# Kernel tuning notes

Hardware: AMD Instinct MI355X
Metric: run time of the kernel (lower is better)

## Reference

```python
import jax, jax.numpy as jnp
import numpy as np
import math

N_VERT = 35709
N_FACE = 70789
BATCH = 32


def _normalize(x, axis=-1, eps=1e-12):
    n = jnp.linalg.norm(x, axis=axis, keepdims=True)
    return x / jnp.maximum(n, eps)


def setup_inputs() -> dict:
    key = jax.random.key(0)
    ks = jax.random.split(key, 9)
    coeff = jax.random.normal(ks[0], (BATCH, 277), jnp.float32)
    idBase = jax.random.normal(ks[1], (3 * N_VERT, 80), jnp.float32)
    exBase = jax.random.normal(ks[2], (3 * N_VERT, 64), jnp.float32)
    texBase = jax.random.normal(ks[3], (3 * N_VERT, 100), jnp.float32)
    meanshape = jax.random.normal(ks[4], (3 * N_VERT,), jnp.float32)
    meantex = jax.random.normal(ks[5], (3 * N_VERT,), jnp.float32)
    face_buf = jax.random.randint(ks[6], (N_FACE, 3), 0, N_VERT, jnp.int32)
    # point_buf may index the appended zero-normal row at position N_FACE (padding)
    point_buf = jax.random.randint(ks[7], (N_VERT, 8), 0, N_FACE + 1, jnp.int32)
    keypoints = jax.random.randint(ks[8], (68,), 0, N_VERT, jnp.int32)
    return dict(coeff=coeff, idBase=idBase, exBase=exBase, texBase=texBase,
                meanshape=meanshape, meantex=meantex, face_buf=face_buf,
                point_buf=point_buf, keypoints=keypoints)


def reference(coeff, idBase, exBase, texBase, meanshape, meantex,
              face_buf, point_buf, keypoints):
    B = coeff.shape[0]
    # ---- Split_coeff (canonical 80/64/100/3/27/3 layout) ----
    id_c = coeff[:, :80]
    ex_c = coeff[:, 80:144]
    tex_c = coeff[:, 144:244]
    angles = coeff[:, 244:247]
    gamma = coeff[:, 247:274]
    trans = coeff[:, 274:277]
    cam_scale = jnp.ones((B, 1), coeff.dtype)
    f_scale = jnp.ones((B, 1), coeff.dtype)

    # ---- Shape formation ----
    fs = (jnp.einsum('ij,aj->ai', idBase, id_c)
          + jnp.einsum('ij,aj->ai', exBase, ex_c)
          + meanshape[None, :])
    fs = fs.reshape(B, -1, 3)  # [B, N, 3]
    fs = fs - jnp.mean(meanshape.reshape(-1, 3), axis=0)[None, None, :]

    # ---- Texture formation ----
    tex = (jnp.einsum('ij,aj->ai', texBase, tex_c) + meantex[None, :]).reshape(B, -1, 3)

    # ---- Rotation matrix (Rz @ Ry @ Rx, then transpose) ----
    cx, sx = jnp.cos(angles[:, 0]), jnp.sin(angles[:, 0])
    cy, sy = jnp.cos(angles[:, 1]), jnp.sin(angles[:, 1])
    cz, sz = jnp.cos(angles[:, 2]), jnp.sin(angles[:, 2])
    o, z = jnp.ones_like(cx), jnp.zeros_like(cx)
    Rx = jnp.stack([o, z, z, z, cx, -sx, z, sx, cx], -1).reshape(B, 3, 3)
    Ry = jnp.stack([cy, z, sy, z, o, z, -sy, z, cy], -1).reshape(B, 3, 3)
    Rz = jnp.stack([cz, -sz, z, sz, cz, z, z, z, o], -1).reshape(B, 3, 3)
    rot = jnp.swapaxes(jnp.matmul(jnp.matmul(Rz, Ry), Rx), 1, 2)  # [B,3,3]

    # ---- Compute_norm: gather face verts, cross, aggregate to vertices ----
    v1 = fs[:, face_buf[:, 0], :]  # [B, F, 3]
    v2 = fs[:, face_buf[:, 1], :]
    v3 = fs[:, face_buf[:, 2], :]
    face_norm = _normalize(jnp.cross(v1 - v2, v2 - v3), axis=2)  # [B, F, 3]
    face_norm = jnp.concatenate(
        [face_norm, jnp.zeros((B, 1, 3), face_norm.dtype)], axis=1)  # pad row
    v_norm = _normalize(jnp.sum(face_norm[:, point_buf, :], axis=2), axis=2)  # [B,N,3]

    norm_r = jnp.matmul(v_norm, rot)

    # ---- Rigid transform + landmarks ----
    fst = jnp.matmul(fs, rot) + trans[:, None, :]
    lm = fst[:, keypoints, :]  # [B, 68, 3]

    # ---- Projection block (applied to landmarks) ----
    focal = 1015.0 * f_scale  # [B,1]
    camera_pos = jnp.array([0.0, 0.0, 10.0], coeff.dtype) * cam_scale[:, :, None]  # [B,1,3]
    reverse_z = jnp.diag(jnp.array([1.0, 1.0, -1.0], coeff.dtype))
    z1 = jnp.zeros((B, 1), coeff.dtype)
    z2 = jnp.zeros((B, 2), coeff.dtype)
    o1 = jnp.ones((B, 1), coeff.dtype)
    p_matrix = jnp.concatenate(
        [focal, z1, 112.0 * o1, z1, focal, 112.0 * o1, z2, o1], axis=1).reshape(B, 3, 3)
    lm_cam = jnp.matmul(lm, reverse_z[None]) + camera_pos
    aug = jnp.matmul(lm_cam, jnp.swapaxes(p_matrix, 1, 2))
    landmark_p = aug[..., :2] / aug[..., 2:3]

    # ---- SH illumination ----
    init_lit = jnp.array([0.8, 0, 0, 0, 0, 0, 0, 0, 0], coeff.dtype)
    g = gamma.reshape(B, 3, 9) + init_lit[None, None, :]
    pi = math.pi
    a0, a1, a2 = pi, 2 * pi / math.sqrt(3.0), 2 * pi / math.sqrt(8.0)
    c0 = 1.0 / math.sqrt(4 * pi)
    c1 = math.sqrt(3.0) / math.sqrt(4 * pi)
    c2 = 3 * math.sqrt(5.0) / math.sqrt(12 * pi)
    nx, ny, nz = norm_r[..., 0], norm_r[..., 1], norm_r[..., 2]
    Y = jnp.stack([
        a0 * c0 * jnp.ones_like(nx),
        -a1 * c1 * ny,
        a1 * c1 * nz,
        -a1 * c1 * nx,
        a2 * c2 * nx * ny,
        -a2 * c2 * ny * nz,
        a2 * c2 * 0.5 / math.sqrt(3.0) * (3 * nz * nz - 1),
        -a2 * c2 * nx * nz,
        a2 * c2 * 0.5 * (nx * nx - ny * ny),
    ], axis=-1)  # [B, N, 9]
    lighting = jnp.einsum('bnk,bck->bnc', Y, g)  # [B, N, 3]
    face_color = tex * lighting

    return face_color, landmark_p, fst
```

## Files before the change

### kernel.cpp

```cpp
#include <hip/hip_runtime.h>

#define N_VERT 35709
#define N_FACE 70789
#define NB 32
#define M3 (3*N_VERT)

#define WS_FS4X  ((size_t)0)
#define WS_FN4X  (WS_FS4X + (size_t)N_VERT*128)
#define WS_CPAD  (WS_FN4X + (size_t)(N_FACE+1)*128)
#define WS_ROT   (WS_CPAD + (size_t)NB*256)
#define WS_TRE   (WS_ROT + (size_t)NB*9)
#define WS_G     (WS_TRE + (size_t)NB*3)
#define WS_MEAN  (WS_G + (size_t)NB*27)

#define FC_OFF   ((size_t)0)
#define LM_OFF   ((size_t)NB*M3)
#define FST_OFF  (LM_OFF + (size_t)NB*68*2)

#define A0C0 0.88622692545275801f
#define A1C1 1.77245385090551603f
#define A2C2 2.42703239430f
#define Y6C  0.70062393935f
#define Y8C  1.21351619715f

__global__ void __launch_bounds__(256) face3d_stageA1(
    const float* __restrict__ ms, float* __restrict__ ws) {
  float s0=0.f, s1=0.f, s2=0.f;
  for (int v = blockIdx.x*256 + threadIdx.x; v < N_VERT; v += gridDim.x*256) {
    s0 += ms[3*v+0]; s1 += ms[3*v+1]; s2 += ms[3*v+2];
  }
  #pragma unroll
  for (int off = 32; off > 0; off >>= 1) {
    s0 += __shfl_down(s0, off);
    s1 += __shfl_down(s1, off);
    s2 += __shfl_down(s2, off);
  }
  if ((threadIdx.x & 63) == 0) {
    atomicAdd(&ws[WS_MEAN+0], s0);
    atomicAdd(&ws[WS_MEAN+1], s1);
    atomicAdd(&ws[WS_MEAN+2], s2);
  }
}

__global__ void __launch_bounds__(256) face3d_stageA2(
    const float* __restrict__ coeff, float* __restrict__ ws) {
  int t = threadIdx.x;
  float m0 = ws[WS_MEAN+0]*(1.0f/N_VERT);
  float m1 = ws[WS_MEAN+1]*(1.0f/N_VERT);
  float m2 = ws[WS_MEAN+2]*(1.0f/N_VERT);
  for (int idx = t; idx < NB*256; idx += 256) {
    int b = idx >> 8, k = idx & 255;
    ws[WS_CPAD + idx] = (k < 244) ? coeff[b*277 + k] : 0.0f;
  }
  for (int idx = t; idx < NB*27; idx += 256) {
    int b = idx / 27, k = idx - b*27;
    ws[WS_G + idx] = coeff[b*277 + 247 + k] + (((k % 9) == 0) ? 0.8f : 0.0f);
  }
  if (t < NB) {
    int b = t;
    float ax = coeff[b*277+244], ay = coeff[b*277+245], az = coeff[b*277+246];
    float cx=cosf(ax), sx=sinf(ax);
    float cy=cosf(ay), sy=sinf(ay);
    float cz=cosf(az), sz=sinf(az);
    float T00=cz*cy, T01=-sz, T02=cz*sy;
    float T10=sz*cy, T11=cz,  T12=sz*sy;
    float T20=-sy,   T21=0.f, T22=cy;
    float R[3][3];
    R[0][0]=T00; R[0][1]=T01*cx+T02*sx; R[0][2]=-T01*sx+T02*cx;
    R[1][0]=T10; R[1][1]=T11*cx+T12*sx; R[1][2]=-T11*sx+T12*cx;
    R[2][0]=T20; R[2][1]=T21*cx+T22*sx; R[2][2]=-T21*sx+T22*cx;
    float rot[3][3];
    #pragma unroll
    for (int c=0;c<3;c++)
      #pragma unroll
      for (int j=0;j<3;j++)
        rot[c][j] = R[j][c];
    #pragma unroll
    for (int c=0;c<3;c++)
      #pragma unroll
      for (int j=0;j<3;j++)
        ws[WS_ROT + b*9 + c*3 + j] = rot[c][j];
    #pragma unroll
    for (int j=0;j<3;j++)
      ws[WS_TRE + b*3 + j] = coeff[b*277+274+j]
        - (m0*rot[0][j] + m1*rot[1][j] + m2*rot[2][j]);
  }
}

template<int NK4, int COFF>
__device__ __forceinline__ void phaseK(const float* __restrict__ Arow,
                                       const float4* __restrict__ Wl,
                                       float* __restrict__ acc) {
  const float4* __restrict__ A = (const float4*)Arow;
  float4 cur = A[0];
  #pragma unroll 1
  for (int s = 0; s < NK4; ++s) {
    float4 a = cur;
    if (s + 1 < NK4) cur = A[s+1];
    #pragma unroll
    for (int b = 0; b < NB; ++b) {
      float4 w = Wl[b*64 + COFF + s];
      acc[b] = fmaf(a.x, w.x, fmaf(a.y, w.y, fmaf(a.z, w.z, fmaf(a.w, w.w, acc[b]))));
    }
  }
}

__global__ void __launch_bounds__(256) face3d_stageB(
    const float* __restrict__ idB, const float* __restrict__ exB,
    const float* __restrict__ texB, const float* __restrict__ meanshape,
    const float* __restrict__ meantex, const float* __restrict__ cpad,
    float* __restrict__ fs4x, float* __restrict__ texOut) {
  __shared__ float4 W[2048];
  int t = threadIdx.x;
  {
    const float4* __restrict__ src = (const float4*)cpad;
    #pragma unroll
    for (int j = 0; j < 8; ++j) W[t + 256*j] = src[t + 256*j];
  }
  __syncthreads();
  int r = blockIdx.x*256 + t;
  if (r >= M3) return;

  float acc[NB];
  #pragma unroll
  for (int b=0;b<NB;b++) acc[b]=0.f;
  phaseK<20, 0 >(idB + (size_t)r*80,  W, acc);
  phaseK<16, 20>(exB + (size_t)r*64,  W, acc);
  {
    float ms = meanshape[r];
    int v = r/3, c = r - 3*v;
    float* dst = fs4x + (size_t)v*128 + c;
    #pragma unroll
    for (int b=0;b<NB;b++) dst[b*4] = acc[b] + ms;
  }
  #pragma unroll
  for (int b=0;b<NB;b++) acc[b]=0.f;
  phaseK<25, 36>(texB + (size_t)r*100, W, acc);
  {
    float mt = meantex[r];
    #pragma unroll
    for (int b=0;b<NB;b++) texOut[(size_t)b*M3 + r] = acc[b] + mt;
  }
}

__global__ void __launch_bounds__(256) face3d_stageC(
    const int* __restrict__ face_buf, const float* __restrict__ fs4x,
    float* __restrict__ fn4x) {
  int t = threadIdx.x;
  int b = t & 31, fi = t >> 5;
  int f = blockIdx.x*8 + fi;
  if (f > N_FACE) return;
  float4* o = (float4*)(fn4x + ((size_t)f*32 + b)*4);
  if (f == N_FACE) { *o = make_float4(0.f,0.f,0.f,0.f); return; }
  int i0 = face_buf[f*3+0];
  int i1 = face_buf[f*3+1];
  int i2 = face_buf[f*3+2];
  float4 p1 = *(const float4*)(fs4x + ((size_t)i0*32 + b)*4);
  float4 p2 = *(const float4*)(fs4x + ((size_t)i1*32 + b)*4);
  float4 p3 = *(const float4*)(fs4x + ((size_t)i2*32 + b)*4);
  float e1x = p1.x-p2.x, e1y = p1.y-p2.y, e1z = p1.z-p2.z;
  float e2x = p2.x-p3.x, e2y = p2.y-p3.y, e2z = p2.z-p3.z;
  float nx = e1y*e2z - e1z*e2y;
  float ny = e1z*e2x - e1x*e2z;
  float nz = e1x*e2y - e1y*e2x;
  float inv = 1.0f / fmaxf(sqrtf(nx*nx + ny*ny + nz*nz), 1e-12f);
  *o = make_float4(nx*inv, ny*inv, nz*inv, 0.f);
}

__global__ void __launch_bounds__(256) face3d_stageD(
    const int* __restrict__ point_buf, const int* __restrict__ keypoints,
    const float* __restrict__ fs4x, const float* __restrict__ fn4x,
    const float* __restrict__ rotAll, const float* __restrict__ treAll,
    const float* __restrict__ gAll, float* __restrict__ out) {
  const int mainBlocks = (N_VERT + 7)/8;
  int bid = blockIdx.x;
  int t = threadIdx.x;
  if (bid < mainBlocks) {
    __shared__ float rotL[NB*9];
    __shared__ float treL[NB*3];
    __shared__ float gL[NB*27];
    __shared__ float fstL[NB*33];
    __shared__ float LL[NB*33];
    if (t < NB*9)  rotL[t] = rotAll[t];
    if (t < NB*3)  treL[t] = treAll[t];
    for (int i = t; i < NB*27; i += 256) gL[i] = gAll[i];
    __syncthreads();
    int b = t & 31, vi = t >> 5;
    int v0 = bid*8;
    int v = v0 + vi;
    if (v < N_VERT) {
      const int4 pb0 = *(const int4*)(point_buf + (size_t)v*8);
      const int4 pb1 = *(const int4*)(point_buf + (size_t)v*8 + 4);
      float4 g0 = *(const float4*)(fn4x + ((size_t)pb0.x*32 + b)*4);
      float4 g1 = *(const float4*)(fn4x + ((size_t)pb0.y*32 + b)*4);
      float4 g2 = *(const float4*)(fn4x + ((size_t)pb0.z*32 + b)*4);
      float4 g3 = *(const float4*)(fn4x + ((size_t)pb0.w*32 + b)*4);
      float4 g4 = *(const float4*)(fn4x + ((size_t)pb1.x*32 + b)*4);
      float4 g5 = *(const float4*)(fn4x + ((size_t)pb1.y*32 + b)*4);
      float4 g6 = *(const float4*)(fn4x + ((size_t)pb1.z*32 + b)*4);
      float4 g7 = *(const float4*)(fn4x + ((size_t)pb1.w*32 + b)*4);
      float sx = ((g0.x+g1.x)+(g2.x+g3.x)) + ((g4.x+g5.x)+(g6.x+g7.x));
      float sy = ((g0.y+g1.y)+(g2.y+g3.y)) + ((g4.y+g5.y)+(g6.y+g7.y));
      float sz = ((g0.z+g1.z)+(g2.z+g3.z)) + ((g4.z+g5.z)+(g6.z+g7.z));
      float inv = 1.0f / fmaxf(sqrtf(sx*sx + sy*sy + sz*sz), 1e-12f);
      float n0 = sx*inv, n1 = sy*inv, n2 = sz*inv;
      const float* rot = rotL + b*9;
      float r00=rot[0], r01=rot[1], r02=rot[2];
      float r10=rot[3], r11=rot[4], r12=rot[5];
      float r20=rot[6], r21=rot[7], r22=rot[8];
      float nx = n0*r00 + n1*r10 + n2*r20;
      float ny = n0*r01 + n1*r11 + n2*r21;
      float nz = n0*r02 + n1*r12 + n2*r22;
      float Y1 = -A1C1*ny;
      float Y2 =  A1C1*nz;
      float Y3 = -A1C1*nx;
      float Y4 =  A2C2*nx*ny;
      float Y5 = -A2C2*ny*nz;
      float Y6 =  Y6C*(3.f*nz*nz - 1.f);
      float Y7 = -A2C2*nx*nz;
      float Y8 =  Y8C*(nx*nx - ny*ny);
      const float* g = gL + b*27;
      #pragma unroll
      for (int c = 0; c < 3; ++c) {
        const float* gc = g + c*9;
        float Lc = A0C0*gc[0] + Y1*gc[1] + Y2*gc[2] + Y3*gc[3] + Y4*gc[4]
                 + Y5*gc[5] + Y6*gc[6] + Y7*gc[7] + Y8*gc[8];
        LL[b*33 + vi*4 + c] = Lc;
      }
      float4 fsv = *(const float4*)(fs4x + ((size_t)v*32 + b)*4);
      const float* tre = treL + b*3;
      fstL[b*33 + vi*4 + 0] = fsv.x*r00 + fsv.y*r10 + fsv.z*r20 + tre[0];
      fstL[b*33 + vi*4 + 1] = fsv.x*r01 + fsv.y*r11 + fsv.z*r21 + tre[1];
      fstL[b*33 + vi*4 + 2] = fsv.x*r02 + fsv.y*r12 + fsv.z*r22 + tre[2];
    }
    __syncthreads();
    int b2 = t >> 3, w = t & 7;
    if (v0 + w < N_VERT) {
      size_t obase = (size_t)b2*M3 + (size_t)(v0 + w)*3;
      float f0 = fstL[b2*33 + w*4 + 0];
      float f1 = fstL[b2*33 + w*4 + 1];
      float f2 = fstL[b2*33 + w*4 + 2];
      out[FST_OFF + obase + 0] = f0;
      out[FST_OFF + obase + 1] = f1;
      out[FST_OFF + obase + 2] = f2;
      float l0 = LL[b2*33 + w*4 + 0];
      float l1 = LL[b2*33 + w*4 + 1];
      float l2 = LL[b2*33 + w*4 + 2];
      float t0 = out[FC_OFF + obase + 0];
      float t1 = out[FC_OFF + obase + 1];
      float t2 = out[FC_OFF + obase + 2];
      out[FC_OFF + obase + 0] = t0*l0;
      out[FC_OFF + obase + 1] = t1*l1;
      out[FC_OFF + obase + 2] = t2*l2;
    }
  } else {
    int idx = (bid - mainBlocks)*256 + t;
    if (idx >= NB*68) return;
    int b = idx & 31, j = idx >> 5;
    int kp = keypoints[j];
    const float* rot = rotAll + b*9;
    const float* tre = treAll + b*3;
    float4 fsv = *(const float4*)(fs4x + ((size_t)kp*32 + b)*4);
    float o0 = fsv.x*rot[0] + fsv.y*rot[3] + fsv.z*rot[6] + tre[0];
    float o1 = fsv.x*rot[1] + fsv.y*rot[4] + fsv.z*rot[7] + tre[1];
    float o2 = fsv.x*rot[2] + fsv.y*rot[5] + fsv.z*rot[8] + tre[2];
    float zc = 10.0f - o2;
    float axv = 1015.0f*o0 + 112.0f*zc;
    float ayv = 1015.0f*o1 + 112.0f*zc;
    out[LM_OFF + (size_t)b*136 + (size_t)j*2 + 0] = axv/zc;
    out[LM_OFF + (size_t)b*136 + (size_t)j*2 + 1] = ayv/zc;
  }
}

extern "C" void kernel_launch(void* const* d_in, const int* in_sizes, int n_in,
                              void* d_out, int out_size, void* d_ws, size_t ws_size,
                              hipStream_t stream) {
  const float* coeff     = (const float*)d_in[0];
  const float* idB       = (const float*)d_in[1];
  const float* exB       = (const float*)d_in[2];
  const float* texB      = (const float*)d_in[3];
  const float* meanshape = (const float*)d_in[4];
  const float* meantex   = (const float*)d_in[5];
  const int*   face_buf  = (const int*)d_in[6];
  const int*   point_buf = (const int*)d_in[7];
  const int*   keypoints = (const int*)d_in[8];
  float* out = (float*)d_out;
  float* ws  = (float*)d_ws;

  hipMemsetAsync((char*)d_ws + WS_MEAN*sizeof(float), 0, 3*sizeof(float), stream);

  hipLaunchKernelGGL(face3d_stageA1, dim3(56), dim3(256), 0, stream, meanshape, ws);
  hipLaunchKernelGGL(face3d_stageA2, dim3(1), dim3(256), 0, stream, coeff, ws);

  int gridB = (M3 + 255)/256;
  hipLaunchKernelGGL(face3d_stageB, dim3(gridB), dim3(256), 0, stream,
                     idB, exB, texB, meanshape, meantex,
                     ws + WS_CPAD, ws + WS_FS4X, out + FC_OFF);

  int gridC = (N_FACE + 1 + 7)/8;
  hipLaunchKernelGGL(face3d_stageC, dim3(gridC), dim3(256), 0, stream,
                     face_buf, ws + WS_FS4X, ws + WS_FN4X);

  int mainBlocks = (N_VERT + 7)/8;
  int lmBlocks   = (NB*68 + 255)/256;
  hipLaunchKernelGGL(face3d_stageD, dim3(mainBlocks + lmBlocks), dim3(256), 0, stream,
                     point_buf, keypoints, ws + WS_FS4X, ws + WS_FN4X,
                     ws + WS_ROT, ws + WS_TRE, ws + WS_G, out);
}
```

Baseline: 286.5 us.

## Stream basis rows through double-buffered LDS with async global-to-LDS loads

Stage B is restructured so each block stages tiles of the basis matrices and coefficients into double-buffered LDS using global_load_lds, with explicit vmcnt waits and barriers. Each thread now computes a 4-row by 8-batch register tile instead of one row across all 32 batches. Shape (id+ex) and texture work are split across separate blocks, which doubles the grid. The intent is coalesced, overlapped streaming of the roughly 100 MB of basis data and more parallelism, in exchange for hand-tuned waitcnt logic that is fragile.

```diff
diff --git a/kernel.cpp b/kernel.cpp
--- a/kernel.cpp
+++ b/kernel.cpp
@@ -87,20 +87,57 @@
   }
 }
 
-template<int NK4, int COFF>
-__device__ __forceinline__ void phaseK(const float* __restrict__ Arow,
-                                       const float4* __restrict__ Wl,
-                                       float* __restrict__ acc) {
-  const float4* __restrict__ A = (const float4*)Arow;
-  float4 cur = A[0];
-  #pragma unroll 1
-  for (int s = 0; s < NK4; ++s) {
-    float4 a = cur;
-    if (s + 1 < NK4) cur = A[s+1];
-    #pragma unroll
-    for (int b = 0; b < NB; ++b) {
-      float4 w = Wl[b*64 + COFF + s];
-      acc[b] = fmaf(a.x, w.x, fmaf(a.y, w.y, fmaf(a.z, w.z, fmaf(a.w, w.w, acc[b]))));
+
+__device__ __forceinline__ void gload16(const void* g, void* l) {
+  __builtin_amdgcn_global_load_lds((const __attribute__((address_space(1))) void*)g,
+                                   (__attribute__((address_space(3))) void*)l, 16, 0, 0);
+}
+
+#define B_SYNC() do { __builtin_amdgcn_sched_barrier(0); \
+                      __builtin_amdgcn_s_barrier(); \
+                      __builtin_amdgcn_sched_barrier(0); } while (0)
+#define B_WAIT(N) do { __builtin_amdgcn_sched_barrier(0); \
+                       asm volatile("s_waitcnt vmcnt(" #N ")"); \
+                       B_SYNC(); } while (0)
+
+template<int KT4>
+__device__ __forceinline__ void stageB_stage(const float* __restrict__ A, int K4,
+                                             int gk4, const float* __restrict__ cpad,
+                                             int wk4, int r0, int t,
+                                             float4* __restrict__ buf) {
+  #pragma unroll
+  for (int p = 0; p < KT4; ++p) {
+    int i = p*256 + t;
+    int row = i / KT4;
+    int s4 = i - row*KT4;
+    int gr = r0 + row; gr = (gr < M3) ? gr : (M3-1);
+    gload16(A + ((size_t)gr*K4 + gk4 + s4)*4, buf + i);
+  }
+  {
+    int b = t / KT4;
+    int s4 = t - b*KT4;
+    if (b >= NB) { b = NB-1; s4 = KT4-1; }
+    gload16(cpad + ((size_t)b*64 + wk4 + s4)*4, buf + 256*KT4 + t);
+  }
+}
+
+template<int KT4>
+__device__ __forceinline__ void stageB_compute(const float4* __restrict__ buf,
+                                               int bg8, int lane, float acc[4][8]) {
+  const float4* __restrict__ Wl = buf + 256*KT4;
+  #pragma unroll
+  for (int s4 = 0; s4 < KT4; ++s4) {
+    float4 a0 = buf[(lane      )*KT4 + s4];
+    float4 a1 = buf[(lane +  64)*KT4 + s4];
+    float4 a2 = buf[(lane + 128)*KT4 + s4];
+    float4 a3 = buf[(lane + 192)*KT4 + s4];
+    #pragma unroll
+    for (int bb = 0; bb < 8; ++bb) {
+      float4 w = Wl[(bg8 + bb)*KT4 + s4];
+      acc[0][bb] = fmaf(a0.w, w.w, fmaf(a0.z, w.z, fmaf(a0.y, w.y, fmaf(a0.x, w.x, acc[0][bb]))));
+      acc[1][bb] = fmaf(a1.w, w.w, fmaf(a1.z, w.z, fmaf(a1.y, w.y, fmaf(a1.x, w.x, acc[1][bb]))));
+      acc[2][bb] = fmaf(a2.w, w.w, fmaf(a2.z, w.z, fmaf(a2.y, w.y, fmaf(a2.x, w.x, acc[2][bb]))));
+      acc[3][bb] = fmaf(a3.w, w.w, fmaf(a3.z, w.z, fmaf(a3.y, w.y, fmaf(a3.x, w.x, acc[3][bb]))));
     }
   }
 }
@@ -110,36 +147,80 @@
     const float* __restrict__ texB, const float* __restrict__ meanshape,
     const float* __restrict__ meantex, const float* __restrict__ cpad,
     float* __restrict__ fs4x, float* __restrict__ texOut) {
-  __shared__ float4 W[2048];
+  __shared__ float4 lds[2][1536];
   int t = threadIdx.x;
-  {
-    const float4* __restrict__ src = (const float4*)cpad;
-    #pragma unroll
-    for (int j = 0; j < 8; ++j) W[t + 256*j] = src[t + 256*j];
-  }
-  __syncthreads();
-  int r = blockIdx.x*256 + t;
-  if (r >= M3) return;
-
-  float acc[NB];
+  int lane = t & 63;
+  int bg8 = (t >> 6) << 3;
+  int bid = blockIdx.x;
+  int r0 = (bid >> 1) * 256;
+
+  float acc[4][8];
   #pragma unroll
-  for (int b=0;b<NB;b++) acc[b]=0.f;
-  phaseK<20, 0 >(idB + (size_t)r*80,  W, acc);
-  phaseK<16, 20>(exB + (size_t)r*64,  W, acc);
-  {
-    float ms = meanshape[r];
-    int v = r/3, c = r - 3*v;
-    float* dst = fs4x + (size_t)v*128 + c;
-    #pragma unroll
-    for (int b=0;b<NB;b++) dst[b*4] = acc[b] + ms;
-  }
-  #pragma unroll
-  for (int b=0;b<NB;b++) acc[b]=0.f;
-  phaseK<25, 36>(texB + (size_t)r*100, W, acc);
-  {
-    float mt = meantex[r];
-    #pragma unroll
-    for (int b=0;b<NB;b++) texOut[(size_t)b*M3 + r] = acc[b] + mt;
+  for (int j = 0; j < 4; ++j)
+    #pragma unroll
+    for (int bb = 0; bb < 8; ++bb) acc[j][bb] = 0.f;
+
+  float4* buf0 = &lds[0][0];
+  float4* buf1 = &lds[1][0];
+
+  if ((bid & 1) == 0) {
+    stageB_stage<5>(idB, 20, 0, cpad, 0, r0, t, buf0);
+    #pragma unroll 1
+    for (int tt = 0; tt < 7; ++tt) {
+      int nt = tt + 1;
+      float4* nb = (tt & 1) ? buf0 : buf1;
+      if (nt < 7) {
+        const float* An = (nt < 4) ? idB : exB;
+        int K4n = (nt < 4) ? 20 : 16;
+        int g4n = (nt < 4) ? nt*5 : (nt-4)*5;
+        stageB_stage<5>(An, K4n, g4n, cpad, nt*5, r0, t, nb);
+        B_WAIT(6);
+      } else {
+        stageB_stage<1>(exB, 16, 15, cpad, 35, r0, t, nb);
+        B_WAIT(2);
+      }
+      stageB_compute<5>((tt & 1) ? buf1 : buf0, bg8, lane, acc);
+      B_SYNC();
+    }
+    B_WAIT(0);
+    stageB_compute<1>(buf1, bg8, lane, acc);
+    #pragma unroll
+    for (int j = 0; j < 4; ++j) {
+      int r = r0 + lane + 64*j;
+      if (r < M3) {
+        float ms = meanshape[r];
+        int v = r / 3;
+        int c = r - 3*v;
+        float* dst = fs4x + (size_t)v*128 + c;
+        #pragma unroll
+        for (int bb = 0; bb < 8; ++bb)
+          dst[(bg8 + bb)*4] = acc[j][bb] + ms;
+      }
+    }
+  } else {
+    stageB_stage<5>(texB, 25, 0, cpad, 36, r0, t, buf0);
+    #pragma unroll 1
+    for (int tt = 0; tt < 5; ++tt) {
+      if (tt < 4) {
+        stageB_stage<5>(texB, 25, (tt+1)*5, cpad, 36 + (tt+1)*5, r0, t,
+                        (tt & 1) ? buf0 : buf1);
+        B_WAIT(6);
+      } else {
+        B_WAIT(0);
+      }
+      stageB_compute<5>((tt & 1) ? buf1 : buf0, bg8, lane, acc);
+      if (tt < 4) B_SYNC();
+    }
+    #pragma unroll
+    for (int j = 0; j < 4; ++j) {
+      int r = r0 + lane + 64*j;
+      if (r < M3) {
+        float mt = meantex[r];
+        #pragma unroll
+        for (int bb = 0; bb < 8; ++bb)
+          texOut[(size_t)(bg8 + bb)*M3 + r] = acc[j][bb] + mt;
+      }
+    }
   }
 }
 
@@ -292,7 +373,7 @@
   hipLaunchKernelGGL(face3d_stageA1, dim3(56), dim3(256), 0, stream, meanshape, ws);
   hipLaunchKernelGGL(face3d_stageA2, dim3(1), dim3(256), 0, stream, coeff, ws);
 
-  int gridB = (M3 + 255)/256;
+  int gridB = 2 * ((M3 + 255)/256);
   hipLaunchKernelGGL(face3d_stageB, dim3(gridB), dim3(256), 0, stream,
                      idB, exB, texB, meanshape, meantex,
                      ws + WS_CPAD, ws + WS_FS4X, out + FC_OFF);
```

New measurement: 289.0 us. About the same (+0.9%).

## Split stage B GEMV into shape/tex blocks with 4-way K-split per row

Applied to the files above, without the earlier changes.

Stage B now runs separate blocks for the shape (id+ex) and texture products. Within a block, each group of four threads splits the K dimension of one output row, and partial sums are combined with two rounds of xor shuffles so each lane writes 8 batch outputs. The aim is more blocks and waves in flight, shorter per-thread dependent loops, and more coalesced base-matrix reads. In exchange it adds shuffle traffic, and the shared weight table is reloaded by every block.

```diff
diff --git a/kernel.cpp b/kernel.cpp
--- a/kernel.cpp
+++ b/kernel.cpp
@@ -87,59 +87,110 @@
   }
 }
 
-template<int NK4, int COFF>
-__device__ __forceinline__ void phaseK(const float* __restrict__ Arow,
-                                       const float4* __restrict__ Wl,
-                                       float* __restrict__ acc) {
-  const float4* __restrict__ A = (const float4*)Arow;
-  float4 cur = A[0];
-  #pragma unroll 1
-  for (int s = 0; s < NK4; ++s) {
-    float4 a = cur;
-    if (s + 1 < NK4) cur = A[s+1];
-    #pragma unroll
-    for (int b = 0; b < NB; ++b) {
-      float4 w = Wl[b*64 + COFF + s];
-      acc[b] = fmaf(a.x, w.x, fmaf(a.y, w.y, fmaf(a.z, w.z, fmaf(a.w, w.w, acc[b]))));
-    }
-  }
-}
 
 __global__ void __launch_bounds__(256) face3d_stageB(
     const float* __restrict__ idB, const float* __restrict__ exB,
     const float* __restrict__ texB, const float* __restrict__ meanshape,
     const float* __restrict__ meantex, const float* __restrict__ cpad,
     float* __restrict__ fs4x, float* __restrict__ texOut) {
-  __shared__ float4 W[2048];
+  __shared__ float4 Wl[NB*36];
   int t = threadIdx.x;
-  {
-    const float4* __restrict__ src = (const float4*)cpad;
-    #pragma unroll
-    for (int j = 0; j < 8; ++j) W[t + 256*j] = src[t + 256*j];
+  int bid = blockIdx.x;
+  int isTex = bid & 1;
+  int r0 = (bid >> 1) * 64;
+  int rl = t >> 2, q = t & 3;
+  int r = r0 + rl;
+  int rc = (r < M3) ? r : (M3-1);
+
+  const float4* __restrict__ cp4 = (const float4*)cpad;
+  if (!isTex) {
+    for (int i = t; i < NB*36; i += 256) {
+      int b = i / 36, j = i - b*36;
+      Wl[i] = cp4[b*64 + j];
+    }
+  } else {
+    for (int i = t; i < NB*25; i += 256) {
+      int b = i / 25, j = i - b*25;
+      Wl[i] = cp4[b*64 + 36 + j];
+    }
   }
   __syncthreads();
-  int r = blockIdx.x*256 + t;
-  if (r >= M3) return;
 
   float acc[NB];
   #pragma unroll
-  for (int b=0;b<NB;b++) acc[b]=0.f;
-  phaseK<20, 0 >(idB + (size_t)r*80,  W, acc);
-  phaseK<16, 20>(exB + (size_t)r*64,  W, acc);
-  {
-    float ms = meanshape[r];
-    int v = r/3, c = r - 3*v;
-    float* dst = fs4x + (size_t)v*128 + c;
-    #pragma unroll
-    for (int b=0;b<NB;b++) dst[b*4] = acc[b] + ms;
-  }
+  for (int b = 0; b < NB; ++b) acc[b] = 0.f;
+
+  if (!isTex) {
+    const float4* __restrict__ Aid = (const float4*)idB + (size_t)rc*20 + 5*q;
+    const float4* __restrict__ Aex = (const float4*)exB + (size_t)rc*16 + 4*q;
+    int kid = 5*q;
+    int kex = 20 + 4*q;
+    #pragma unroll
+    for (int s = 0; s < 5; ++s) {
+      float4 a = Aid[s];
+      #pragma unroll
+      for (int b = 0; b < NB; ++b) {
+        float4 w = Wl[b*36 + kid + s];
+        acc[b] = fmaf(a.w, w.w, fmaf(a.z, w.z, fmaf(a.y, w.y, fmaf(a.x, w.x, acc[b]))));
+      }
+    }
+    #pragma unroll
+    for (int s = 0; s < 4; ++s) {
+      float4 a = Aex[s];
+      #pragma unroll
+      for (int b = 0; b < NB; ++b) {
+        float4 w = Wl[b*36 + kex + s];
+        acc[b] = fmaf(a.w, w.w, fmaf(a.z, w.z, fmaf(a.y, w.y, fmaf(a.x, w.x, acc[b]))));
+      }
+    }
+  } else {
+    int toff = (q == 0) ? 0 : (6*q + 1);
+    int tlen = 6 + (q == 0);
+    const float4* __restrict__ At = (const float4*)texB + (size_t)rc*25 + toff;
+    #pragma unroll
+    for (int s = 0; s < 7; ++s) {
+      if (s < tlen) {
+        float4 a = At[s];
+        #pragma unroll
+        for (int b = 0; b < NB; ++b) {
+          float4 w = Wl[b*25 + toff + s];
+          acc[b] = fmaf(a.w, w.w, fmaf(a.z, w.z, fmaf(a.y, w.y, fmaf(a.x, w.x, acc[b]))));
+        }
+      }
+    }
+  }
+
+  int q1 = q & 1, q2 = q & 2;
+  float half16[16];
   #pragma unroll
-  for (int b=0;b<NB;b++) acc[b]=0.f;
-  phaseK<25, 36>(texB + (size_t)r*100, W, acc);
-  {
-    float mt = meantex[r];
-    #pragma unroll
-    for (int b=0;b<NB;b++) texOut[(size_t)b*M3 + r] = acc[b] + mt;
+  for (int b = 0; b < 16; ++b) {
+    float send = q1 ? acc[b] : acc[b+16];
+    float keep = q1 ? acc[b+16] : acc[b];
+    half16[b] = keep + __shfl_xor(send, 1);
+  }
+  float fin[8];
+  #pragma unroll
+  for (int b = 0; b < 8; ++b) {
+    float send = q2 ? half16[b] : half16[b+8];
+    float keep = q2 ? half16[b+8] : half16[b];
+    fin[b] = keep + __shfl_xor(send, 2);
+  }
+  int bb0 = q1*16 + q2*4;
+
+  if (r < M3) {
+    if (!isTex) {
+      float msv = meanshape[r];
+      int v = r/3, c = r - 3*v;
+      float* dst = fs4x + (size_t)v*128 + c + bb0*4;
+      #pragma unroll
+      for (int bb = 0; bb < 8; ++bb)
+        dst[bb*4] = fin[bb] + msv;
+    } else {
+      float mtv = meantex[r];
+      #pragma unroll
+      for (int bb = 0; bb < 8; ++bb)
+        texOut[(size_t)(bb0 + bb)*M3 + r] = fin[bb] + mtv;
+    }
   }
 }
 
@@ -292,7 +343,7 @@
   hipLaunchKernelGGL(face3d_stageA1, dim3(56), dim3(256), 0, stream, meanshape, ws);
   hipLaunchKernelGGL(face3d_stageA2, dim3(1), dim3(256), 0, stream, coeff, ws);
 
-  int gridB = (M3 + 255)/256;
+  int gridB = 2 * ((M3 + 63)/64);
   hipLaunchKernelGGL(face3d_stageB, dim3(gridB), dim3(256), 0, stream,
                      idB, exB, texB, meanshape, meantex,
                      ws + WS_CPAD, ws + WS_FS4X, out + FC_OFF);
```

Measured after the change: 348.9 us. 1.22x slower.

## Split shape and texture GEMV into separate blocks, read coefficients from global

Applied to the files above, without the earlier changes.

Stage B now launches twice as many blocks. Even blocks compute the shape basis product and odd blocks compute the texture product, so they run concurrently instead of one after the other in each thread. The shared-memory staging of coefficients and its barrier are removed. Coefficients are stored transposed as [k4][batch] float4 and read directly from global memory, which the code expects to be uniform, cache-resident loads. This adds parallelism and occupancy, at the cost of relying on cache or scalar loads for the weight reads in place of LDS.

```diff
diff --git a/kernel.cpp b/kernel.cpp
--- a/kernel.cpp
+++ b/kernel.cpp
@@ -48,9 +48,16 @@
   float m0 = ws[WS_MEAN+0]*(1.0f/N_VERT);
   float m1 = ws[WS_MEAN+1]*(1.0f/N_VERT);
   float m2 = ws[WS_MEAN+2]*(1.0f/N_VERT);
-  for (int idx = t; idx < NB*256; idx += 256) {
-    int b = idx >> 8, k = idx & 255;
-    ws[WS_CPAD + idx] = (k < 244) ? coeff[b*277 + k] : 0.0f;
+  float4* cp4 = (float4*)(ws + WS_CPAD);
+  for (int idx = t; idx < 64*32; idx += 256) {
+    int s4 = idx >> 5, b = idx & 31;
+    int k = 4*s4;
+    float4 v;
+    v.x = (k < 244) ? coeff[b*277 + k + 0] : 0.f;
+    v.y = (k < 244) ? coeff[b*277 + k + 1] : 0.f;
+    v.z = (k < 244) ? coeff[b*277 + k + 2] : 0.f;
+    v.w = (k < 244) ? coeff[b*277 + k + 3] : 0.f;
+    cp4[idx] = v;
   }
   for (int idx = t; idx < NB*27; idx += 256) {
     int b = idx / 27, k = idx - b*27;
@@ -87,20 +94,21 @@
   }
 }
 
-template<int NK4, int COFF>
-__device__ __forceinline__ void phaseK(const float* __restrict__ Arow,
-                                       const float4* __restrict__ Wl,
-                                       float* __restrict__ acc) {
-  const float4* __restrict__ A = (const float4*)Arow;
+
+template<int NK4, int SOFF>
+__device__ __forceinline__ void phaseKs(const float4* __restrict__ A,
+                                        const float4* __restrict__ W,
+                                        float* __restrict__ acc) {
   float4 cur = A[0];
   #pragma unroll 1
   for (int s = 0; s < NK4; ++s) {
     float4 a = cur;
     if (s + 1 < NK4) cur = A[s+1];
+    const float4* __restrict__ Ws = W + (size_t)(SOFF + s)*32;
     #pragma unroll
     for (int b = 0; b < NB; ++b) {
-      float4 w = Wl[b*64 + COFF + s];
-      acc[b] = fmaf(a.x, w.x, fmaf(a.y, w.y, fmaf(a.z, w.z, fmaf(a.w, w.w, acc[b]))));
+      float4 w = Ws[b];
+      acc[b] = fmaf(a.w, w.w, fmaf(a.z, w.z, fmaf(a.y, w.y, fmaf(a.x, w.x, acc[b]))));
     }
   }
 }
@@ -108,38 +116,32 @@
 __global__ void __launch_bounds__(256) face3d_stageB(
     const float* __restrict__ idB, const float* __restrict__ exB,
     const float* __restrict__ texB, const float* __restrict__ meanshape,
-    const float* __restrict__ meantex, const float* __restrict__ cpad,
+    const float* __restrict__ meantex, const float* __restrict__ cpadT,
     float* __restrict__ fs4x, float* __restrict__ texOut) {
-  __shared__ float4 W[2048];
   int t = threadIdx.x;
-  {
-    const float4* __restrict__ src = (const float4*)cpad;
-    #pragma unroll
-    for (int j = 0; j < 8; ++j) W[t + 256*j] = src[t + 256*j];
-  }
-  __syncthreads();
-  int r = blockIdx.x*256 + t;
+  int bid = blockIdx.x;
+  int isTex = bid & 1;
+  int r = (bid >> 1)*256 + t;
   if (r >= M3) return;
+  const float4* __restrict__ W = (const float4*)cpadT;
 
   float acc[NB];
   #pragma unroll
-  for (int b=0;b<NB;b++) acc[b]=0.f;
-  phaseK<20, 0 >(idB + (size_t)r*80,  W, acc);
-  phaseK<16, 20>(exB + (size_t)r*64,  W, acc);
-  {
-    float ms = meanshape[r];
+  for (int b = 0; b < NB; ++b) acc[b] = 0.f;
+
+  if (!isTex) {
+    phaseKs<20, 0 >((const float4*)idB + (size_t)r*20, W, acc);
+    phaseKs<16, 20>((const float4*)exB + (size_t)r*16, W, acc);
+    float msv = meanshape[r];
     int v = r/3, c = r - 3*v;
     float* dst = fs4x + (size_t)v*128 + c;
     #pragma unroll
-    for (int b=0;b<NB;b++) dst[b*4] = acc[b] + ms;
-  }
-  #pragma unroll
-  for (int b=0;b<NB;b++) acc[b]=0.f;
-  phaseK<25, 36>(texB + (size_t)r*100, W, acc);
-  {
-    float mt = meantex[r];
-    #pragma unroll
-    for (int b=0;b<NB;b++) texOut[(size_t)b*M3 + r] = acc[b] + mt;
+    for (int b = 0; b < NB; ++b) dst[b*4] = acc[b] + msv;
+  } else {
+    phaseKs<25, 36>((const float4*)texB + (size_t)r*25, W, acc);
+    float mtv = meantex[r];
+    #pragma unroll
+    for (int b = 0; b < NB; ++b) texOut[(size_t)b*M3 + r] = acc[b] + mtv;
   }
 }
 
@@ -292,7 +294,7 @@
   hipLaunchKernelGGL(face3d_stageA1, dim3(56), dim3(256), 0, stream, meanshape, ws);
   hipLaunchKernelGGL(face3d_stageA2, dim3(1), dim3(256), 0, stream, coeff, ws);
 
-  int gridB = (M3 + 255)/256;
+  int gridB = 2 * ((M3 + 255)/256);
   hipLaunchKernelGGL(face3d_stageB, dim3(gridB), dim3(256), 0, stream,
                      idB, exB, texB, meanshape, meantex,
                      ws + WS_CPAD, ws + WS_FS4X, out + FC_OFF);
```

Result: no change. 291.5 us (+1.8%).
